# Kernel optimization log

Measured on AMD Instinct MI355X. Metric: run time of the kernel, lower is better.

## Reference

```python
import jax, jax.numpy as jnp
import numpy as np

H = 2048            # hidden_size
HK, HV = 16, 32     # num_k_heads, num_v_heads
DK, DV = 128, 128   # head dims
KEY_DIM = HK * DK   # 2048
VAL_DIM = HV * DV   # 4096
CONV_DIM = 2 * KEY_DIM + VAL_DIM  # 8192
KW = 4              # conv kernel width
CS = 64             # chunk size
B, S = 2, 4096
EPS = 1e-6


def setup_inputs() -> dict:
    key = jax.random.key(0)
    ks = jax.random.split(key, 8)
    sc = lambda n: 1.0 / np.sqrt(n)
    return {
        "hidden_states": jax.random.normal(ks[0], (B, S, H), jnp.float32),
        "W_qkvz": jax.random.normal(ks[1], (H, 2 * KEY_DIM + 2 * VAL_DIM), jnp.float32) * sc(H),
        "W_ba": jax.random.normal(ks[2], (H, 2 * HV), jnp.float32) * sc(H),
        "conv_w": jax.random.normal(ks[3], (CONV_DIM, KW), jnp.float32) * sc(KW),
        "A_log": jnp.log(jax.random.uniform(ks[4], (HV,), jnp.float32, 1.0, 16.0)),
        "dt_bias": jax.random.normal(ks[5], (HV,), jnp.float32) * 0.1,
        "norm_weight": jnp.ones((DV,), jnp.float32),
        "W_out": jax.random.normal(ks[6], (VAL_DIM, H), jnp.float32) * sc(VAL_DIM),
    }


def l2norm(x, eps=1e-6):
    return x * jax.lax.rsqrt(jnp.sum(x * x, -1, keepdims=True) + eps)


def chunk_gated_delta_rule(q, k, v, g, beta):
    # q,k: (B,S,HV,DK); v: (B,S,HV,DV); g,beta: (B,S,HV). S divisible by CS.
    q = l2norm(q)
    k = l2norm(k)
    tr = lambda x: jnp.swapaxes(x, 1, 2).astype(jnp.float32)  # -> (B,H,S,...)
    q, k, v = tr(q), tr(k), tr(v)
    g = jnp.swapaxes(g, 1, 2).astype(jnp.float32)
    beta = jnp.swapaxes(beta, 1, 2).astype(jnp.float32)
    q = q * (1.0 / np.sqrt(DK))
    nc = S // CS
    rs = lambda x: x.reshape(B, HV, nc, CS, x.shape[-1])
    v_beta = v * beta[..., None]
    k_beta = k * beta[..., None]
    q, k, v, k_beta, v_beta = map(rs, (q, k, v, k_beta, v_beta))
    g = jnp.cumsum(g.reshape(B, HV, nc, CS), -1)
    tril = jnp.tril(jnp.ones((CS, CS), bool))
    diff = g[..., :, None] - g[..., None, :]
    decay = jnp.exp(jnp.where(tril, diff, 0.0)) * tril  # (B,H,nc,CS,CS)
    # strictly-lower A; the original sequential loop computes T = (I - A)^{-1}
    A = -jnp.tril(jnp.einsum('bhcid,bhcjd->bhcij', k_beta, k) * decay, -1)
    eye = jnp.eye(CS, dtype=jnp.float32)
    T = jax.scipy.linalg.solve_triangular(
        eye - A, jnp.broadcast_to(eye, A.shape), lower=True, unit_diagonal=True)
    v_t = jnp.einsum('bhcij,bhcjd->bhcid', T, v_beta)
    k_cumdecay = jnp.einsum('bhcij,bhcjd->bhcid', T, k_beta * jnp.exp(g)[..., None])
    strict_low = jnp.tril(jnp.ones((CS, CS), jnp.float32), -1)

    def step(state, xs):
        q_i, k_i, v_i, kc_i, g_i, dm_i = xs  # (B,H,CS,*)
        attn = jnp.einsum('bhid,bhjd->bhij', q_i, k_i) * dm_i * strict_low
        v_new = v_i - kc_i @ state
        out = (q_i * jnp.exp(g_i)[..., None]) @ state + attn @ v_new
        g_last = g_i[..., -1]
        state = state * jnp.exp(g_last)[..., None, None] + jnp.einsum(
            'bhcd,bhcv->bhdv', k_i * jnp.exp(g_last[..., None] - g_i)[..., None], v_new)
        return state, out

    S0 = jnp.zeros((B, HV, DK, DV), jnp.float32)
    mv = lambda x: jnp.moveaxis(x, 2, 0)  # chunk axis first for scan
    _, outs = jax.lax.scan(step, S0, (mv(q), mv(k), mv(v_t), mv(k_cumdecay), mv(g), mv(decay)))
    out = jnp.moveaxis(outs, 0, 2).reshape(B, HV, S, DV)
    return jnp.swapaxes(out, 1, 2)  # (B,S,HV,DV)


def reference(hidden_states, W_qkvz, W_ba, conv_w, A_log, dt_bias, norm_weight, W_out):
    r = HV // HK
    qkvz = hidden_states @ W_qkvz                     # (B,S,2*KEY+2*VAL)
    ba = hidden_states @ W_ba                         # (B,S,2*HV)
    qkvz = qkvz.reshape(B, S, HK, 2 * DK + 2 * r * DV)
    q, k, v, z = jnp.split(qkvz, [DK, 2 * DK, 2 * DK + r * DV], axis=-1)
    v = v.reshape(B, S, HV, DV)
    z = z.reshape(B, S, HV, DV)
    ba = ba.reshape(B, S, HK, 2 * r)
    b, a = jnp.split(ba, [r], axis=-1)
    b = b.reshape(B, S, HV)
    a = a.reshape(B, S, HV)
    # fused causal depthwise conv + silu over [q|k|v]
    mixed = jnp.concatenate([q.reshape(B, S, -1), k.reshape(B, S, -1), v.reshape(B, S, -1)], -1)
    x = jnp.swapaxes(mixed, 1, 2)                     # (B, CONV_DIM, S)
    xp = jnp.pad(x, ((0, 0), (0, 0), (KW - 1, 0)))
    conv = sum(conv_w[:, j][None, :, None] * xp[:, :, j:j + S] for j in range(KW))
    conv = jax.nn.silu(conv)
    qkv = jnp.swapaxes(conv, 1, 2)
    q, k, v = jnp.split(qkv, [KEY_DIM, 2 * KEY_DIM], axis=-1)
    q = q.reshape(B, S, HK, DK)
    k = k.reshape(B, S, HK, DK)
    v = v.reshape(B, S, HV, DV)
    beta = jax.nn.sigmoid(b)
    g = -jnp.exp(A_log) * jax.nn.softplus(a + dt_bias)
    q = jnp.repeat(q, r, axis=2)
    k = jnp.repeat(k, r, axis=2)
    core = chunk_gated_delta_rule(q, k, v, g, beta)   # (B,S,HV,DV)
    # gated RMSNorm over head_v_dim
    cf = core.astype(jnp.float32)
    var = jnp.mean(cf * cf, -1, keepdims=True)
    core = cf * jax.lax.rsqrt(var + EPS) * norm_weight
    core = core * jax.nn.silu(z.astype(jnp.float32))
    return core.reshape(B, S, VAL_DIM) @ W_out        # (B,S,H)
```

## Files before the change

### kernel.cpp

```cpp
#include <hip/hip_runtime.h>
#include <cstdint>
#include <cstddef>


typedef _Float16 half_t;
typedef _Float16 half2_t __attribute__((ext_vector_type(2)));
typedef _Float16 half4_t __attribute__((ext_vector_type(4)));
typedef _Float16 half8   __attribute__((ext_vector_type(8)));
typedef float    f32x4   __attribute__((ext_vector_type(4)));

#define MFMA16(a, b, c) __builtin_amdgcn_mfma_f32_16x16x32_f16((a), (b), (c), 0, 0, 0)

#define AS1 __attribute__((address_space(1)))
#define AS3 __attribute__((address_space(3)))

__device__ __forceinline__ void gload16(void* lds, const void* g) {
    __builtin_amdgcn_global_load_lds((AS1 void*)(g), (AS3 void*)(lds), 16, 0, 0);
}

__device__ __forceinline__ void at_wr(float* AT, int i, int j, float v) {
    *(float*)((char*)AT + i * 256 + ((j * 4) ^ ((i & 7) << 4))) = v;
}
__device__ __forceinline__ half8 frag64(const half_t* base, int row, int koff) {
    return *(const half8*)((const char*)base + row * 128 + ((koff * 2) ^ ((row & 7) << 4)));
}
__device__ __forceinline__ void w64(half_t* base, int row, int col, float v) {
    *(half_t*)((char*)base + row * 128 + ((col * 2) ^ ((row & 7) << 4))) = (half_t)v;
}
__device__ __forceinline__ half8 frag128(const half_t* base, int row, int koff) {
    return *(const half8*)((const char*)base + row * 256 + ((koff * 2) ^ ((row & 7) << 4)));
}

__global__ __launch_bounds__(256) void cast_h_k(const float* __restrict__ src,
                                                half_t* __restrict__ dst) {
    const long n4 = (long)8192 * 2048 / 4;
    for (long i = (long)blockIdx.x * 256 + threadIdx.x; i < n4; i += (long)gridDim.x * 256) {
        f32x4 v = *(const f32x4*)(src + i * 4);
        half4_t h;
        h[0] = (half_t)v[0]; h[1] = (half_t)v[1]; h[2] = (half_t)v[2]; h[3] = (half_t)v[3];
        *(half4_t*)(dst + i * 4) = h;
    }
}

__global__ __launch_bounds__(256) void build_w1t_k(const float* __restrict__ Wq,
                                                   const float* __restrict__ Wba,
                                                   half_t* __restrict__ W1T) {
    __shared__ half_t tile[32][33];
    int n0 = blockIdx.x * 32, k0 = blockIdx.y * 32;
    int tx = threadIdx.x & 31, ty = threadIdx.x >> 5;
#pragma unroll
    for (int t = 0; t < 4; ++t) {
        int k = k0 + ty + t * 8, n = n0 + tx;
        float v = 0.f;
        if (n < 2048) {
            int kh = n >> 7, d = n & 127;
            v = Wq[(long)k * 12288 + kh * 768 + d];
        } else if (n < 4096) {
            int n2 = n - 2048; int kh = n2 >> 7, d = n2 & 127;
            v = Wq[(long)k * 12288 + kh * 768 + 128 + d];
        } else if (n < 8192) {
            int n3 = n - 4096; int vh = n3 >> 7, d = n3 & 127;
            int kh = vh >> 1, jj = vh & 1;
            v = Wq[(long)k * 12288 + kh * 768 + 256 + jj * 128 + d];
        } else if (n < 8256) {
            v = Wba[(long)k * 64 + (n - 8192)];
        } else if (n >= 8448) {
            int n4 = n - 8448; int vh = n4 >> 7, d = n4 & 127;
            int kh = vh >> 1, jj = vh & 1;
            v = Wq[(long)k * 12288 + kh * 768 + 512 + jj * 128 + d];
        }
        tile[ty + t * 8][tx] = (half_t)v;
    }
    __syncthreads();
#pragma unroll
    for (int t = 0; t < 4; ++t) {
        int n = n0 + ty + t * 8, k = k0 + tx;
        W1T[(long)n * 2048 + k] = tile[tx][ty + t * 8];
    }
}

__global__ __launch_bounds__(256) void build_wot_k(const float* __restrict__ Wo,
                                                   half_t* __restrict__ WoT) {
    __shared__ half_t tile[32][33];
    int n0 = blockIdx.x * 32, k0 = blockIdx.y * 32;
    int tx = threadIdx.x & 31, ty = threadIdx.x >> 5;
#pragma unroll
    for (int t = 0; t < 4; ++t) {
        int k = k0 + ty + t * 8, n = n0 + tx;
        tile[ty + t * 8][tx] = (half_t)Wo[(long)k * 2048 + n];
    }
    __syncthreads();
#pragma unroll
    for (int t = 0; t < 4; ++t) {
        int n = n0 + ty + t * 8, k = k0 + tx;
        WoT[(long)n * 4096 + k] = tile[tx][ty + t * 8];
    }
}

template <int OUT_F16>
__global__ __launch_bounds__(512, 2) void gemm256_k(const half_t* __restrict__ A,
                                                    const half_t* __restrict__ Bt,
                                                    void* __restrict__ C,
                                                    int K, int ldc,
                                                    int nwgM, int nwgN) {
    __shared__ half_t LA[2][2][8192];
    __shared__ half_t LB[2][2][8192];
    const int tid = threadIdx.x, lane = tid & 63, w = tid >> 6;
    const int lo = lane & 15, hi = lane >> 4;
    const int wm = w >> 2, wn = w & 3;
    const int nwg = gridDim.x, q = nwg >> 3, bid = blockIdx.x;
    const int swz = (bid & 7) * q + (bid >> 3);
    const int grp = 8 * nwgN;
    const int gid = swz / grp;
    const int rem = swz - gid * grp;
    const int fm = gid * 8;
    const int gsz = min(nwgM - fm, 8);
    const long tm = fm + rem % gsz;
    const long tn = rem / gsz;
    const long Kb = (long)K * 2;
    const char* Ab = (const char*)A + tm * 256 * Kb;
    const char* Bb = (const char*)Bt + tn * 256 * Kb;
    const int scol = ((lane & 7) << 4) ^ ((lane >> 3) << 4);
    const int srow = lane >> 3;
    const int s0 = w * 2, s1 = w * 2 + 1;

    auto stA = [&](int kt, int h) {
        char* hb = (char*)&LA[kt & 1][h][0];
        const char* gb = Ab + (long)(h * 128) * Kb + (long)kt * 128;
        gload16(hb + s0 * 1024, gb + (long)(s0 * 8 + srow) * Kb + scol);
        gload16(hb + s1 * 1024, gb + (long)(s1 * 8 + srow) * Kb + scol);
    };
    auto stB = [&](int kt, int h) {
        char* hb = (char*)&LB[kt & 1][h][0];
        const char* gb = Bb + (long)(h * 128) * Kb + (long)kt * 128;
        gload16(hb + s0 * 1024, gb + (long)(s0 * 8 + srow) * Kb + scol);
        gload16(hb + s1 * 1024, gb + (long)(s1 * 8 + srow) * Kb + scol);
    };
    auto rdA = [&](int p, int mt, int ks) -> half8 {
        int r = mt * 16 + lo;
        return *(const half8*)((const char*)&LA[p][wm][0] + r * 128 +
                               ((ks * 64 + hi * 16) ^ ((r & 7) << 4)));
    };
    auto rdB = [&](int p, int nt, int ks) -> half8 {
        int r = (wn & 1) * 64 + nt * 16 + lo;
        return *(const half8*)((const char*)&LB[p][wn >> 1][0] + r * 128 +
                               ((ks * 64 + hi * 16) ^ ((r & 7) << 4)));
    };

    f32x4 acc[8][4] = {};
    half8 af[4][2], bfa[2][2], bfb[2][2];

    auto ldsA4 = [&](int p, int mbase) {
#pragma unroll
        for (int mt = 0; mt < 4; ++mt) {
            af[mt][0] = rdA(p, mbase + mt, 0);
            af[mt][1] = rdA(p, mbase + mt, 1);
        }
    };
    auto ldsB2 = [&](int p, int nbase, half8 (&dst)[2][2]) {
#pragma unroll
        for (int nt = 0; nt < 2; ++nt) {
            dst[nt][0] = rdB(p, nbase + nt, 0);
            dst[nt][1] = rdB(p, nbase + nt, 1);
        }
    };
    auto quad = [&](const half8 (&bq)[2][2], int mo, int no) {
        __builtin_amdgcn_s_setprio(1);
#pragma unroll
        for (int mt = 0; mt < 4; ++mt)
#pragma unroll
            for (int nt = 0; nt < 2; ++nt) {
                acc[mo + mt][no + nt] = MFMA16(af[mt][0], bq[nt][0], acc[mo + mt][no + nt]);
                acc[mo + mt][no + nt] = MFMA16(af[mt][1], bq[nt][1], acc[mo + mt][no + nt]);
            }
        __builtin_amdgcn_s_setprio(0);
        __builtin_amdgcn_s_barrier();
    };

    const int nkt = K >> 6, niter = nkt >> 1;
    stA(0, 0); stA(0, 1); stB(0, 0); stB(0, 1);
    stA(1, 0); stB(1, 0); stB(1, 1);
    asm volatile("s_waitcnt vmcnt(6)" ::: "memory");
    __builtin_amdgcn_s_barrier();
    ldsB2(0, 0, bfa);

    for (int i = 0; i < niter; ++i) {
        const int k0 = 2 * i, k1 = 2 * i + 1;
        const bool sa = (k0 + 2 < nkt), sb = (k1 + 2 < nkt);
        ldsA4(0, 0);
        stA(k1, 1);
        __builtin_amdgcn_s_barrier();
        quad(bfa, 0, 0);
        ldsB2(0, 2, bfb);
        __builtin_amdgcn_s_barrier();
        quad(bfb, 0, 2);
        ldsA4(0, 4);
        if (sa) stB(k0 + 2, 0);
        __builtin_amdgcn_s_barrier();
        quad(bfa, 4, 0);
        if (sa) {
            stA(k0 + 2, 0); stB(k0 + 2, 1);
            asm volatile("s_waitcnt vmcnt(6)" ::: "memory");
        } else {
            asm volatile("s_waitcnt vmcnt(0)" ::: "memory");
        }
        ldsB2(1, 0, bfa);
        __builtin_amdgcn_s_barrier();
        quad(bfb, 4, 2);
        ldsA4(1, 0);
        if (sa) stA(k0 + 2, 1);
        __builtin_amdgcn_s_barrier();
        quad(bfa, 0, 0);
        ldsB2(1, 2, bfb);
        __builtin_amdgcn_s_barrier();
        quad(bfb, 0, 2);
        ldsA4(1, 4);
        if (sb) stB(k1 + 2, 0);
        __builtin_amdgcn_s_barrier();
        quad(bfa, 4, 0);
        if (sb) {
            stA(k1 + 2, 0); stB(k1 + 2, 1);
            asm volatile("s_waitcnt vmcnt(6)" ::: "memory");
        }
        if (i + 1 < niter) ldsB2(0, 0, bfa);
        __builtin_amdgcn_s_barrier();
        quad(bfb, 4, 2);
    }

    const long crow0 = tm * 256 + wm * 128 + hi * 4;
    const long ccol0 = tn * 256 + wn * 64 + lo;
#pragma unroll
    for (int mt = 0; mt < 8; ++mt)
#pragma unroll
        for (int nt = 0; nt < 4; ++nt)
#pragma unroll
            for (int e = 0; e < 4; ++e) {
                long row = crow0 + mt * 16 + e;
                long col = ccol0 + nt * 16;
                if (OUT_F16)
                    ((half_t*)C)[row * (long)ldc + col] = (half_t)acc[mt][nt][e];
                else
                    ((float*)C)[row * (long)ldc + col] = acc[mt][nt][e];
            }
}

__global__ __launch_bounds__(256) void conv_silu_k(const half_t* __restrict__ mixedH,
                                                   const float* __restrict__ conv_w,
                                                   half_t* __restrict__ qb,
                                                   half_t* __restrict__ kb,
                                                   half_t* __restrict__ vb) {
    const int ldm = 8448;
    int bx = blockIdx.x;
    int ch0 = (bx * 256 + threadIdx.x) * 8;
    int b = blockIdx.y >> 7, sc = blockIdx.y & 127;
    int s0 = sc * 32;
    half_t* dptr;
    long dstr;
    float nsc = 1.f;
    bool donorm = (bx < 2);
    if (bx == 0)      { dptr = qb + ch0;          dstr = 2048; nsc = 0.08838834764831845f; }
    else if (bx == 1) { dptr = kb + (ch0 - 2048); dstr = 2048; }
    else              { dptr = vb + (ch0 - 4096); dstr = 4096; }
    float w0[8], w1[8], w2[8], w3[8];
#pragma unroll
    for (int j = 0; j < 8; ++j) {
        f32x4 wv = *(const f32x4*)(conv_w + (ch0 + j) * 4);
        w0[j] = wv[0]; w1[j] = wv[1]; w2[j] = wv[2]; w3[j] = wv[3];
    }
    const half_t* src = mixedH + (long)b * 4096 * ldm + ch0;
    half8 x0 = {}, x1 = {}, x2 = {};
    if (s0 >= 3) {
        x0 = *(const half8*)(src + (long)(s0 - 3) * ldm);
        x1 = *(const half8*)(src + (long)(s0 - 2) * ldm);
        x2 = *(const half8*)(src + (long)(s0 - 1) * ldm);
    }
    for (int s = s0; s < s0 + 32; ++s) {
        half8 x3 = *(const half8*)(src + (long)s * ldm);
        float y[8];
        float ss = 0.f;
#pragma unroll
        for (int j = 0; j < 8; ++j) {
            float t = w0[j] * (float)x0[j] + w1[j] * (float)x1[j] +
                      w2[j] * (float)x2[j] + w3[j] * (float)x3[j];
            t = t / (1.f + __expf(-t));
            y[j] = t;
            ss += t * t;
        }
        half8 yv;
        if (donorm) {
            ss += __shfl_xor(ss, 1);
            ss += __shfl_xor(ss, 2);
            ss += __shfl_xor(ss, 4);
            ss += __shfl_xor(ss, 8);
            float r = rsqrtf(ss + 1e-6f) * nsc;
#pragma unroll
            for (int j = 0; j < 8; ++j) yv[j] = (half_t)(y[j] * r);
        } else {
#pragma unroll
            for (int j = 0; j < 8; ++j) yv[j] = (half_t)y[j];
        }
        *(half8*)(dptr + ((long)b * 4096 + s) * dstr) = yv;
        x0 = x1; x1 = x2; x2 = x3;
    }
}

__global__ __launch_bounds__(256) void gate_beta_k(const half_t* __restrict__ mixedH,
                                                   const float* __restrict__ A_log,
                                                   const float* __restrict__ dt_bias,
                                                   float* __restrict__ beta,
                                                   float* __restrict__ gcum) {
    __shared__ float gs[32][64];
    int b = blockIdx.x >> 6, c = blockIdx.x & 63;
    for (int idx = threadIdx.x; idx < 2048; idx += 256) {
        int vh = idx & 31, i = idx >> 5;
        int kh = vh >> 1, j = vh & 1;
        long row = ((long)b * 4096 + c * 64 + i) * 8448 + 8192 + kh * 4;
        float bb = (float)mixedH[row + j];
        float aa = (float)mixedH[row + 2 + j];
        beta[((long)b * 4096 + c * 64 + i) * 32 + vh] = 1.f / (1.f + __expf(-bb));
        float x = aa + dt_bias[vh];
        float sp = (x > 15.f) ? x : log1pf(__expf(x));
        gs[vh][i] = -__expf(A_log[vh]) * sp;
    }
    __syncthreads();
    if (threadIdx.x < 32) {
        int vh = threadIdx.x;
        float cum = 0.f;
        float* gout = gcum + ((long)(b * 32 + vh)) * 4096 + c * 64;
        for (int i = 0; i < 64; ++i) { cum += gs[vh][i]; gout[i] = cum; }
    }
}

__global__ __launch_bounds__(256) void phase1_k(const half_t* __restrict__ qb,
                                                const half_t* __restrict__ kb,
                                                const half_t* __restrict__ vb,
                                                const float* __restrict__ beta,
                                                const float* __restrict__ gcum,
                                                half_t* __restrict__ attnW,
                                                half_t* __restrict__ vtW,
                                                half_t* __restrict__ kcW) {
    __shared__ float AT[64 * 64];
    __shared__ half_t XT[256 * 64];
    __shared__ float gcS[64], betaS[64], egS[64];
    int blk = blockIdx.x;
    int c = blk & 63, vh = (blk >> 6) & 31, b = blk >> 11;
    int kh = vh >> 1;
    int tid = threadIdx.x, lane = tid & 63, w = tid >> 6, lo = lane & 15, hi = lane >> 4;
    long rowbase = (long)b * 4096 + c * 64;
    if (tid < 64) {
        float g = gcum[((long)(b * 32 + vh)) * 4096 + c * 64 + tid];
        gcS[tid] = g; egS[tid] = __expf(g);
        betaS[tid] = beta[(rowbase + tid) * 32 + vh];
    }
    const half_t* kR = kb + rowbase * 2048 + kh * 128;
    const half_t* qR = qb + rowbase * 2048 + kh * 128;
    f32x4 accG[4] = {}, accA[4] = {};
#pragma unroll
    for (int kt = 0; kt < 4; ++kt) {
        half8 ak = *(const half8*)(kR + (long)(w * 16 + lo) * 2048 + kt * 32 + hi * 8);
        half8 aq = *(const half8*)(qR + (long)(w * 16 + lo) * 2048 + kt * 32 + hi * 8);
#pragma unroll
        for (int n = 0; n < 4; ++n) {
            half8 bk = *(const half8*)(kR + (long)(n * 16 + lo) * 2048 + kt * 32 + hi * 8);
            accG[n] = MFMA16(ak, bk, accG[n]);
            accA[n] = MFMA16(aq, bk, accA[n]);
        }
    }
    __syncthreads();
    half_t* attnB = attnW + (long)blk * 4096;
#pragma unroll
    for (int n = 0; n < 4; ++n)
#pragma unroll
        for (int e = 0; e < 4; ++e) {
            int i = w * 16 + hi * 4 + e;
            int j = n * 16 + lo;
            float dec = (j < i) ? __expf(gcS[i] - gcS[j]) : 0.f;
            float av = (j < i) ? (-betaS[i] * accG[n][e] * dec) : (j == i ? 1.f : 0.f);
            at_wr(AT, i, j, av);
            attnB[(long)i * 64 + j] = (half_t)((j < i) ? accA[n][e] * dec : 0.f);
        }
    __syncthreads();
    if (w == 0) {
        float t[64];
#pragma unroll
        for (int i = 0; i < 64; ++i) t[i] = (lane == i) ? 1.f : 0.f;
#pragma unroll
        for (int i = 1; i < 64; ++i) {
            float a0 = 0.f, a1 = 0.f, a2 = 0.f, a3 = 0.f;
#pragma unroll
            for (int p0 = 0; p0 < i; p0 += 4) {
                f32x4 a4 = *(const f32x4*)((const char*)AT + i * 256 +
                                           ((p0 * 4) ^ ((i & 7) << 4)));
                if (p0 + 0 < i) a0 += a4[0] * t[p0 + 0];
                if (p0 + 1 < i) a1 += a4[1] * t[p0 + 1];
                if (p0 + 2 < i) a2 += a4[2] * t[p0 + 2];
                if (p0 + 3 < i) a3 += a4[3] * t[p0 + 3];
            }
            t[i] += (a0 + a1) + (a2 + a3);
        }
        half_t* TS = (half_t*)AT;
#pragma unroll
        for (int i = 0; i < 64; ++i)
            *(half_t*)((char*)TS + i * 128 + ((lane * 2) ^ ((i & 7) << 4))) = (half_t)t[i];
    } else {
        for (int idx = tid - 64; idx < 4096; idx += 192) {
            int p = idx >> 6, dp = idx & 63;
            float bb = betaS[p], be = betaS[p] * egS[p];
            half2_t vv = *(const half2_t*)(vb + (rowbase + p) * 4096 + vh * 128 + dp * 2);
            half2_t kk = *(const half2_t*)(kb + (rowbase + p) * 2048 + kh * 128 + dp * 2);
            w64(XT, dp * 2,       p, (float)vv[0] * bb);
            w64(XT, dp * 2 + 1,   p, (float)vv[1] * bb);
            w64(XT, 128 + dp * 2,     p, (float)kk[0] * be);
            w64(XT, 128 + dp * 2 + 1, p, (float)kk[1] * be);
        }
    }
    __syncthreads();
    const half_t* TS = (const half_t*)AT;
    f32x4 accO[4][4] = {};
#pragma unroll
    for (int kt = 0; kt < 2; ++kt) {
        half8 tf[4];
#pragma unroll
        for (int m = 0; m < 4; ++m) tf[m] = frag64(TS, m * 16 + lo, kt * 32 + hi * 8);
#pragma unroll
        for (int n = 0; n < 4; ++n) {
            half8 bx = frag64(XT, w * 64 + n * 16 + lo, kt * 32 + hi * 8);
#pragma unroll
            for (int m = 0; m < 4; ++m) accO[m][n] = MFMA16(tf[m], bx, accO[m][n]);
        }
    }
    long ob = (long)blk * 8192;
#pragma unroll
    for (int m = 0; m < 4; ++m)
#pragma unroll
        for (int n = 0; n < 4; ++n)
#pragma unroll
            for (int e = 0; e < 4; ++e) {
                int i = m * 16 + hi * 4 + e;
                int dc = w * 64 + n * 16 + lo;
                float v = accO[m][n][e];
                if (dc < 128) vtW[ob + (long)i * 128 + dc] = (half_t)v;
                else          kcW[ob + (long)i * 128 + dc - 128] = (half_t)(-v);
            }
}

struct P2Ops {
    half8 kcf[4], qf[4], k8[4];
    half8 atf[2];
    half_t vtv[8];
    float gm, gi, g63;
};

__global__ __launch_bounds__(256, 1) void phase2_k(const half_t* __restrict__ qb,
                                                   const half_t* __restrict__ kb,
                                                   const float* __restrict__ gcum,
                                                   const half_t* __restrict__ attnW,
                                                   const half_t* __restrict__ vtW,
                                                   const half_t* __restrict__ kcW,
                                                   half_t* __restrict__ coreH) {
    __shared__ half_t SHs[32 * 128];
    __shared__ half_t vnT[32 * 64];
    __shared__ half_t kdT[128 * 64];
    int blk = blockIdx.x;
    int bvh = blk & 63, js = blk >> 6;
    int vh = bvh & 31, b = bvh >> 5, kh = vh >> 1;
    int j0 = js * 32;
    int tid = threadIdx.x, lane = tid & 63, w = tid >> 6, lo = lane & 15, hi = lane >> 4;
    int ii = tid >> 2, dseg = tid & 3;
    int jm = w >> 1, dql = (w & 1) * 4;
    for (int idx = tid; idx < 32 * 128; idx += 256) SHs[idx] = (half_t)0.f;
    __syncthreads();
    const float* gbase = gcum + (long)bvh * 4096;

    auto loadops = [&](int c, P2Ops& o) {
        long pb = (long)bvh * 64 + c;
        const half_t* kcG = kcW + pb * 8192;
        const half_t* vtG = vtW + pb * 8192;
        const half_t* atG = attnW + pb * 4096;
        long rowbase = (long)b * 4096 + c * 64;
        const float* gp = gbase + c * 64;
#pragma unroll
        for (int kt = 0; kt < 4; ++kt) {
            o.kcf[kt] = *(const half8*)(kcG + (long)(w * 16 + lo) * 128 + kt * 32 + hi * 8);
            o.qf[kt] = *(const half8*)(qb + (rowbase + w * 16 + lo) * 2048 + kh * 128 +
                                       kt * 32 + hi * 8);
        }
#pragma unroll
        for (int kt2 = 0; kt2 < 2; ++kt2)
            o.atf[kt2] = *(const half8*)(atG + (long)(w * 16 + lo) * 64 + kt2 * 32 + hi * 8);
#pragma unroll
        for (int s = 0; s < 4; ++s)
            o.k8[s] = *(const half8*)(kb + (rowbase + ii) * 2048 + kh * 128 + dseg * 32 + s * 8);
#pragma unroll
        for (int n = 0; n < 2; ++n)
#pragma unroll
            for (int e = 0; e < 4; ++e)
                o.vtv[n * 4 + e] = vtG[(long)(w * 16 + hi * 4 + e) * 128 + j0 + n * 16 + lo];
        o.gm = gp[w * 16 + lo];
        o.gi = gp[ii];
        o.g63 = gp[63];
    };

    auto step = [&](int c, P2Ops& o, P2Ops& nx) {
        long rowbase = (long)b * 4096 + c * 64;
        loadops(c + 1 < 64 ? c + 1 : 63, nx);
        half8 bS[4][2];
#pragma unroll
        for (int kt = 0; kt < 4; ++kt) {
            bS[kt][0] = frag128(SHs, lo, kt * 32 + hi * 8);
            bS[kt][1] = frag128(SHs, 16 + lo, kt * 32 + hi * 8);
        }
        f32x4 accV[2];
#pragma unroll
        for (int n = 0; n < 2; ++n)
#pragma unroll
            for (int e = 0; e < 4; ++e) accV[n][e] = (float)o.vtv[n * 4 + e];
#pragma unroll
        for (int kt = 0; kt < 4; ++kt) {
            accV[0] = MFMA16(o.kcf[kt], bS[kt][0], accV[0]);
            accV[1] = MFMA16(o.kcf[kt], bS[kt][1], accV[1]);
        }
#pragma unroll
        for (int n = 0; n < 2; ++n) {
            int j = n * 16 + lo, i0 = w * 16 + hi * 4;
            half4_t h4;
            h4[0] = (half_t)accV[n][0]; h4[1] = (half_t)accV[n][1];
            h4[2] = (half_t)accV[n][2]; h4[3] = (half_t)accV[n][3];
            *(half4_t*)((char*)vnT + j * 128 + ((i0 * 2) ^ ((j & 7) << 4))) = h4;
        }
        {
            float ek = __expf(o.g63 - o.gi);
#pragma unroll
            for (int s = 0; s < 4; ++s)
#pragma unroll
                for (int e2 = 0; e2 < 8; ++e2)
                    w64(kdT, dseg * 32 + s * 8 + e2, ii, (float)o.k8[s][e2] * ek);
        }
        __syncthreads();
        float egm = __expf(o.gm);
        f32x4 accO[2] = {};
#pragma unroll
        for (int kt = 0; kt < 4; ++kt) {
            half8 aq;
#pragma unroll
            for (int e2 = 0; e2 < 8; ++e2) aq[e2] = (half_t)((float)o.qf[kt][e2] * egm);
            accO[0] = MFMA16(aq, bS[kt][0], accO[0]);
            accO[1] = MFMA16(aq, bS[kt][1], accO[1]);
        }
#pragma unroll
        for (int kt2 = 0; kt2 < 2; ++kt2) {
            half8 bV0 = frag64(vnT, lo, kt2 * 32 + hi * 8);
            half8 bV1 = frag64(vnT, 16 + lo, kt2 * 32 + hi * 8);
            accO[0] = MFMA16(o.atf[kt2], bV0, accO[0]);
            accO[1] = MFMA16(o.atf[kt2], bV1, accO[1]);
        }
        f32x4 accU[4] = {};
#pragma unroll
        for (int kt2 = 0; kt2 < 2; ++kt2) {
            half8 avn = frag64(vnT, jm * 16 + lo, kt2 * 32 + hi * 8);
#pragma unroll
            for (int dnn = 0; dnn < 4; ++dnn) {
                half8 bkd = frag64(kdT, (dql + dnn) * 16 + lo, kt2 * 32 + hi * 8);
                accU[dnn] = MFMA16(avn, bkd, accU[dnn]);
            }
        }
#pragma unroll
        for (int n = 0; n < 2; ++n)
#pragma unroll
            for (int e = 0; e < 4; ++e)
                coreH[(rowbase + w * 16 + hi * 4 + e) * 4096 + vh * 128 + j0 + n * 16 + lo] =
                    (half_t)accO[n][e];
        __syncthreads();
        float egl = __expf(o.g63);
#pragma unroll
        for (int dnn = 0; dnn < 4; ++dnn)
#pragma unroll
            for (int e = 0; e < 4; ++e) {
                int j = jm * 16 + hi * 4 + e;
                int d = (dql + dnn) * 16 + lo;
                char* p = (char*)SHs + j * 256 + ((d * 2) ^ ((j & 7) << 4));
                float old = (float)*(half_t*)p;
                *(half_t*)p = (half_t)(old * egl + accU[dnn][e]);
            }
        __syncthreads();
    };

    P2Ops opsA, opsB;
    loadops(0, opsA);
    for (int c = 0; c < 64; c += 2) {
        step(c, opsA, opsB);
        step(c + 1, opsB, opsA);
    }
}

__global__ __launch_bounds__(256) void normgate_k(half_t* __restrict__ coreH,
                                                  const half_t* __restrict__ zH,
                                                  const float* __restrict__ norm_w) {
    int w = threadIdx.x >> 6, lane = threadIdx.x & 63;
    float w0 = norm_w[lane * 2], w1 = norm_w[lane * 2 + 1];
    for (long rid = (long)blockIdx.x * 4 + w; rid < 262144; rid += (long)gridDim.x * 4) {
        long bs = rid >> 5;
        int vh = rid & 31;
        half_t* cr = coreH + bs * 4096 + vh * 128;
        half2_t cv = *(half2_t*)(cr + lane * 2);
        float f0 = (float)cv[0], f1 = (float)cv[1];
        float ss = f0 * f0 + f1 * f1;
#pragma unroll
        for (int off = 32; off; off >>= 1) ss += __shfl_xor(ss, off);
        float rs = rsqrtf(ss * (1.f / 128.f) + 1e-6f);
        half2_t zz = *(const half2_t*)(zH + bs * 4096 + vh * 128 + lane * 2);
        float z0 = (float)zz[0], z1 = (float)zz[1];
        float s0 = z0 / (1.f + __expf(-z0)), s1 = z1 / (1.f + __expf(-z1));
        half2_t o;
        o[0] = (half_t)(f0 * rs * w0 * s0);
        o[1] = (half_t)(f1 * rs * w1 * s1);
        *(half2_t*)(cr + lane * 2) = o;
    }
}

extern "C" void kernel_launch(void* const* d_in, const int* in_sizes, int n_in,
                              void* d_out, int out_size, void* d_ws, size_t ws_size,
                              hipStream_t stream) {
    const float* hidden  = (const float*)d_in[0];
    const float* W_qkvz  = (const float*)d_in[1];
    const float* W_ba    = (const float*)d_in[2];
    const float* conv_w  = (const float*)d_in[3];
    const float* A_log   = (const float*)d_in[4];
    const float* dt_bias = (const float*)d_in[5];
    const float* norm_w  = (const float*)d_in[6];
    const float* W_out   = (const float*)d_in[7];
    float* out = (float*)d_out;

    char* ws = (char*)d_ws;
    const size_t MB = 1ull << 20;
    half_t* qb      = (half_t*)(ws + 0);
    half_t* kb      = (half_t*)(ws + 32 * MB);
    half_t* vb      = (half_t*)(ws + 64 * MB);
    float*  betaB   = (float*) (ws + 128 * MB);
    float*  gcum    = (float*) (ws + 129 * MB);
    half_t* WoT     = (half_t*)(ws + 130 * MB);
    half_t* zH      = (half_t*)(ws + 146 * MB);
    half_t* mixedH  = (half_t*)(ws + 210 * MB);
    half_t* attnW   = (half_t*)(ws + 210 * MB);
    half_t* vtW     = (half_t*)(ws + 242 * MB);
    half_t* kcW     = (half_t*)(ws + 306 * MB);
    half_t* hiddenH = (half_t*)(ws + 0);
    half_t* W1T     = (half_t*)(ws + 32 * MB);
    half_t* coreH   = (half_t*)(ws + 64 * MB);
    (void)ws_size; (void)in_sizes; (void)n_in; (void)out_size;

    cast_h_k<<<2048, 256, 0, stream>>>(hidden, hiddenH);
    build_w1t_k<<<dim3(392, 64), 256, 0, stream>>>(W_qkvz, W_ba, W1T);
    build_wot_k<<<dim3(64, 128), 256, 0, stream>>>(W_out, WoT);
    gemm256_k<1><<<1056, 512, 0, stream>>>(hiddenH, W1T, mixedH, 2048, 8448, 32, 33);
    gemm256_k<1><<<512, 512, 0, stream>>>(hiddenH, W1T + (size_t)8448 * 2048, zH,
                                          2048, 4096, 32, 16);
    conv_silu_k<<<dim3(4, 256), 256, 0, stream>>>(mixedH, conv_w, qb, kb, vb);
    gate_beta_k<<<128, 256, 0, stream>>>(mixedH, A_log, dt_bias, betaB, gcum);
    phase1_k<<<4096, 256, 0, stream>>>(qb, kb, vb, betaB, gcum, attnW, vtW, kcW);
    phase2_k<<<256, 256, 0, stream>>>(qb, kb, gcum, attnW, vtW, kcW, coreH);
    normgate_k<<<4096, 256, 0, stream>>>(coreH, zH, norm_w);
    gemm256_k<0><<<256, 512, 0, stream>>>(coreH, WoT, out, 4096, 2048, 32, 8);
}
```

Baseline: 1.223 ms.

## Simplify GEMM main loop to one tile per iteration with two barriers

Replaces the hand-interleaved, twice-unrolled GEMM k-loop (eight barriers per two k-tiles, staggered half-tile global-to-LDS loads) with a simpler loop. Each iteration now computes all four quads, then issues the whole next-next tile load and waits at two barriers. The aim is to cut barrier overhead and let MFMA runs go longer uninterrupted. The cost is that load issue is no longer spread across compute phases, so global-load latency may be hidden less well.

Result: faster. 1.152 ms (-5.8%).

```diff
diff --git a/kernel.cpp b/kernel.cpp
--- a/kernel.cpp
+++ b/kernel.cpp
@@ -136,6 +136,7 @@
         gload16(hb + s0 * 1024, gb + (long)(s0 * 8 + srow) * Kb + scol);
         gload16(hb + s1 * 1024, gb + (long)(s1 * 8 + srow) * Kb + scol);
     };
+    auto stTile = [&](int kt) { stA(kt, 0); stA(kt, 1); stB(kt, 0); stB(kt, 1); };
     auto rdA = [&](int p, int mt, int ks) -> half8 {
         int r = mt * 16 + lo;
         return *(const half8*)((const char*)&LA[p][wm][0] + r * 128 +
@@ -174,57 +175,34 @@
                 acc[mo + mt][no + nt] = MFMA16(af[mt][1], bq[nt][1], acc[mo + mt][no + nt]);
             }
         __builtin_amdgcn_s_setprio(0);
+    };
+
+    const int nkt = K >> 6;
+    stTile(0); stTile(1);
+    asm volatile("s_waitcnt vmcnt(8)" ::: "memory");
+    __builtin_amdgcn_s_barrier();
+    ldsA4(0, 0); ldsB2(0, 0, bfa); ldsB2(0, 2, bfb);
+
+    for (int kt = 0; kt < nkt; ++kt) {
+        const int p = kt & 1;
+        quad(bfa, 0, 0);
+        quad(bfb, 0, 2);
+        ldsA4(p, 4);
+        quad(bfa, 4, 0);
+        quad(bfb, 4, 2);
         __builtin_amdgcn_s_barrier();
-    };
-
-    const int nkt = K >> 6, niter = nkt >> 1;
-    stA(0, 0); stA(0, 1); stB(0, 0); stB(0, 1);
-    stA(1, 0); stB(1, 0); stB(1, 1);
-    asm volatile("s_waitcnt vmcnt(6)" ::: "memory");
-    __builtin_amdgcn_s_barrier();
-    ldsB2(0, 0, bfa);
-
-    for (int i = 0; i < niter; ++i) {
-        const int k0 = 2 * i, k1 = 2 * i + 1;
-        const bool sa = (k0 + 2 < nkt), sb = (k1 + 2 < nkt);
-        ldsA4(0, 0);
-        stA(k1, 1);
+        if (kt + 2 < nkt) {
+            stTile(kt + 2);
+            asm volatile("s_waitcnt vmcnt(8)" ::: "memory");
+        } else if (kt + 1 < nkt) {
+            asm volatile("s_waitcnt vmcnt(0)" ::: "memory");
+        }
         __builtin_amdgcn_s_barrier();
-        quad(bfa, 0, 0);
-        ldsB2(0, 2, bfb);
-        __builtin_amdgcn_s_barrier();
-        quad(bfb, 0, 2);
-        ldsA4(0, 4);
-        if (sa) stB(k0 + 2, 0);
-        __builtin_amdgcn_s_barrier();
-        quad(bfa, 4, 0);
-        if (sa) {
-            stA(k0 + 2, 0); stB(k0 + 2, 1);
-            asm volatile("s_waitcnt vmcnt(6)" ::: "memory");
-        } else {
-            asm volatile("s_waitcnt vmcnt(0)" ::: "memory");
-        }
-        ldsB2(1, 0, bfa);
-        __builtin_amdgcn_s_barrier();
-        quad(bfb, 4, 2);
-        ldsA4(1, 0);
-        if (sa) stA(k0 + 2, 1);
-        __builtin_amdgcn_s_barrier();
-        quad(bfa, 0, 0);
-        ldsB2(1, 2, bfb);
-        __builtin_amdgcn_s_barrier();
-        quad(bfb, 0, 2);
-        ldsA4(1, 4);
-        if (sb) stB(k1 + 2, 0);
-        __builtin_amdgcn_s_barrier();
-        quad(bfa, 4, 0);
-        if (sb) {
-            stA(k1 + 2, 0); stB(k1 + 2, 1);
-            asm volatile("s_waitcnt vmcnt(6)" ::: "memory");
-        }
-        if (i + 1 < niter) ldsB2(0, 0, bfa);
-        __builtin_amdgcn_s_barrier();
-        quad(bfb, 4, 2);
+        if (kt + 1 < nkt) {
+            ldsA4(p ^ 1, 0);
+            ldsB2(p ^ 1, 0, bfa);
+            ldsB2(p ^ 1, 2, bfb);
+        }
     }
 
     const long crow0 = tm * 256 + wm * 128 + hi * 4;
```
